# Performance work log

Measured on AMD Instinct MI355X. Metric: run time of the kernel, lower is better.

## Reference

```python
import jax, jax.numpy as jnp
import numpy as np

d_model = 512


def setup_inputs() -> dict:
    key = jax.random.key(0)
    k1, k2, k3, k4 = jax.random.split(key, 4)
    B, T, d_k = 8, 2048, 64
    scale = 1.0 / np.sqrt(d_model)
    x = jax.random.normal(k1, (B, T, d_model), dtype=jnp.float32)
    Wk = jax.random.normal(k2, (d_model, d_k), dtype=jnp.float32) * scale
    Wq = jax.random.normal(k3, (d_model, d_k), dtype=jnp.float32) * scale
    Wv = jax.random.normal(k4, (d_model, d_k), dtype=jnp.float32) * scale
    return {"x": x, "Wk": Wk, "Wq": Wq, "Wv": Wv}


def reference(x, Wk, Wq, Wv):
    # x: [B,T,C]; W*: [C,d_k]  (torch Linear weight is [d_k,C]; we store transposed)
    k = jnp.einsum('btc,cd->btd', x, Wk)
    q = jnp.einsum('btc,cd->btd', x, Wq)
    v = jnp.einsum('btc,cd->btd', x, Wv)
    d_k = k.shape[-1]
    scores = jnp.einsum('bqd,bkd->bqk', q, k) / jnp.sqrt(jnp.float32(d_k))
    attn = jax.nn.softmax(scores, axis=-1)  # [B,T,T]
    return jnp.einsum('bqk,bkd->bqd', attn, v)
```

## Files before the change

### kernel.cpp

```cpp
#include <hip/hip_runtime.h>
#include <hip/hip_bf16.h>
#include <stdint.h>


typedef short bf16x8 __attribute__((ext_vector_type(8)));
typedef float f32x4 __attribute__((ext_vector_type(4)));

#define MFMA_BF16 __builtin_amdgcn_mfma_f32_16x16x32_bf16

__device__ __forceinline__ unsigned int pk2(float a, float b) {
    __hip_bfloat162 h = __float22bfloat162_rn(float2{a, b});
    union { __hip_bfloat162 h; unsigned int u; } r; r.h = h;
    return r.u;
}

__device__ __forceinline__ uint2 pack4_bf16(float a, float b, float c, float d) {
    uint2 r; r.x = pk2(a, b); r.y = pk2(c, d); return r;
}

__device__ __forceinline__ bf16x8 cvt8(f32x4 a, f32x4 b) {
    union { bf16x8 v; unsigned int u[4]; } r;
    r.u[0] = pk2(a[0], a[1]); r.u[1] = pk2(a[2], a[3]);
    r.u[2] = pk2(b[0], b[1]); r.u[3] = pk2(b[2], b[3]);
    return r.v;
}

__device__ __forceinline__ unsigned short bf1(float a) {
    __hip_bfloat16 h = __float2bfloat16(a);
    union { __hip_bfloat16 h; unsigned short u; } r; r.h = h;
    return r.u;
}

__global__ void prep_kernel(const float* __restrict__ x,
                            const float* __restrict__ Wq,
                            const float* __restrict__ Wk,
                            const float* __restrict__ Wv,
                            unsigned short* __restrict__ xb2,
                            unsigned short* __restrict__ wt2)
{
    if (blockIdx.x < 48) {
        int id = blockIdx.x * 256 + threadIdx.x;
        int c    = id & 15;
        int quad = (id >> 4) & 3;
        int ks   = (id >> 6) & 15;
        int mt   = (id >> 10) & 3;
        int w    = id >> 12;
        const float* src = (w == 0) ? Wq : ((w == 1) ? Wk : Wv);
        const int n  = mt * 16 + c;
        const int k0 = ks * 32 + quad * 8;
        unsigned short* dst = wt2 + (size_t)id * 8;
        #pragma unroll
        for (int j = 0; j < 8; j++)
            dst[j] = bf1(src[(size_t)(k0 + j) * 64 + n]);
        return;
    }
    int i = (blockIdx.x - 48) * 256 + threadIdx.x;
    int tok    = i >> 6;
    int dblock = i & 63;
    f32x4 a = *(const f32x4*)(x + (size_t)i * 8);
    f32x4 b = *(const f32x4*)(x + (size_t)i * 8 + 4);
    int tt = tok >> 4, c = tok & 15;
    int ks = dblock >> 2, quad = dblock & 3;
    size_t chunk = ((size_t)(tt * 16 + ks) * 4 + quad) * 16 + c;
    *(bf16x8*)(xb2 + chunk * 8) = cvt8(a, b);
}

__global__ __launch_bounds__(256, 1) void proj_kernel(
    const unsigned short* __restrict__ xb2, const unsigned short* __restrict__ wt2,
    unsigned short* __restrict__ qg, unsigned short* __restrict__ kg2,
    unsigned short* __restrict__ vg2)
{
    const int lane = threadIdx.x & 63;
    const int c    = lane & 15;
    const int quad = lane >> 4;
    const int wave = threadIdx.x >> 6;
    const int gw   = blockIdx.x * 4 + wave;
    const int w    = gw % 3;
    const int tt   = gw / 3;
    const int t0   = tt * 16;

    f32x4 acc[4];
    #pragma unroll
    for (int i = 0; i < 4; i++) acc[i] = f32x4{0.f, 0.f, 0.f, 0.f};

    const unsigned short* xbase = xb2 + ((size_t)tt * 16 * 64 + lane) * 8;
    const unsigned short* wbase = wt2 + ((size_t)w * 4 * 16 * 64 + lane) * 8;

    #pragma unroll 4
    for (int ks = 0; ks < 16; ks++) {
        bf16x8 xf = *(const bf16x8*)(xbase + (size_t)ks * 64 * 8);
        #pragma unroll
        for (int mt = 0; mt < 4; mt++) {
            bf16x8 wa = *(const bf16x8*)(wbase + ((size_t)mt * 16 + ks) * 64 * 8);
            acc[mt] = MFMA_BF16(wa, xf, acc[mt], 0, 0, 0);
        }
    }

    const int b  = t0 >> 11;
    const int tb = t0 & 2047;

    if (w == 0) {
        unsigned short* base = qg + (size_t)(t0 + c) * 64;
        #pragma unroll
        for (int mt = 0; mt < 4; mt++)
            *(uint2*)(base + mt * 16 + quad * 4) =
                pack4_bf16(acc[mt][0], acc[mt][1], acc[mt][2], acc[mt][3]);
    } else if (w == 1) {
        const int g = tb >> 4;
        #pragma unroll
        for (int mt = 0; mt < 4; mt++) {
            const int h  = mt >> 1;
            const int qk = (mt & 1) * 2 + (quad >> 1);
            size_t chunk = (size_t)b * 16384 + ((size_t)(g * 2 + h) * 4 + qk) * 16 + c;
            *(uint2*)(kg2 + chunk * 8 + (quad & 1) * 4) =
                pack4_bf16(acc[mt][0], acc[mt][1], acc[mt][2], acc[mt][3]);
        }
    } else {
        const int tk = tb + c;
        const int s  = tk >> 5;
        const int qv = (tk >> 3) & 3;
        const int j  = tk & 7;
        #pragma unroll
        for (int mt = 0; mt < 4; mt++) {
            size_t chunk = (size_t)b * 16384 + ((size_t)(s * 4 + mt) * 4 + qv) * 16 + quad * 4;
            unsigned short* dst = vg2 + chunk * 8 + j;
            dst[0]  = bf1(acc[mt][0]);
            dst[8]  = bf1(acc[mt][1]);
            dst[16] = bf1(acc[mt][2]);
            dst[24] = bf1(acc[mt][3]);
        }
    }
}

__global__ __launch_bounds__(256, 1) void attn_kernel(
    const unsigned short* __restrict__ qg, const unsigned short* __restrict__ kg2,
    const unsigned short* __restrict__ vg2, float* __restrict__ out)
{
    __shared__ unsigned short pt[4][2][16 * 136];
    __shared__ float obuf[4][2][16][68];
    __shared__ float lbuf[4][2][16];

    const int lane = threadIdx.x & 63;
    const int wave = threadIdx.x >> 6;
    const int c    = lane & 15;
    const int quad = lane >> 4;
    const int b    = blockIdx.x & 7;
    const int g    = blockIdx.x >> 3;
    const int tb   = b * 2048 + g * 32;

    unsigned short* ptw = &pt[wave][0][0];
    const unsigned short* kbase = kg2 + ((size_t)b * 16384 + lane) * 8;
    const unsigned short* vbase = vg2 + ((size_t)b * 16384 + lane) * 8;

    bf16x8 qa0 = *(const bf16x8*)(qg + (size_t)(tb + c) * 64 + quad * 8);
    bf16x8 qa1 = *(const bf16x8*)(qg + (size_t)(tb + c) * 64 + 32 + quad * 8);
    bf16x8 qc0 = *(const bf16x8*)(qg + (size_t)(tb + 16 + c) * 64 + quad * 8);
    bf16x8 qc1 = *(const bf16x8*)(qg + (size_t)(tb + 16 + c) * 64 + 32 + quad * 8);

    f32x4 oa0 = {0,0,0,0}, oa1 = {0,0,0,0}, oa2 = {0,0,0,0}, oa3 = {0,0,0,0};
    f32x4 ob0 = {0,0,0,0}, ob1 = {0,0,0,0}, ob2 = {0,0,0,0}, ob3 = {0,0,0,0};
    f32x4 laccA = {0,0,0,0}, laccB = {0,0,0,0};
    const float cexp = 0.18033688011112042f;

    for (int kt = wave * 4; kt < wave * 4 + 4; kt++) {
        const int key0 = kt * 128;
        const int g0   = key0 >> 4;
        const int s0   = key0 >> 5;

        f32x4 stA[8], stB[8];
        const f32x4 z = {0,0,0,0};
        #pragma unroll
        for (int mt = 0; mt < 8; mt++) {
            bf16x8 k0 = *(const bf16x8*)(kbase + (size_t)((g0 + mt) * 2    ) * 64 * 8);
            bf16x8 k1 = *(const bf16x8*)(kbase + (size_t)((g0 + mt) * 2 + 1) * 64 * 8);
            stA[mt] = MFMA_BF16(k0, qa0, z, 0, 0, 0);
            stA[mt] = MFMA_BF16(k1, qa1, stA[mt], 0, 0, 0);
            stB[mt] = MFMA_BF16(k0, qc0, z, 0, 0, 0);
            stB[mt] = MFMA_BF16(k1, qc1, stB[mt], 0, 0, 0);
        }

        bf16x8 va[2][4];
        #pragma unroll
        for (int mt = 0; mt < 4; mt++) {
            va[0][mt] = *(const bf16x8*)(vbase + (size_t)((s0    ) * 4 + mt) * 64 * 8);
            va[1][mt] = *(const bf16x8*)(vbase + (size_t)((s0 + 1) * 4 + mt) * 64 * 8);
        }

        asm volatile("" ::: "memory");
        #pragma unroll
        for (int mt = 0; mt < 8; mt++) {
            float p0 = __builtin_amdgcn_exp2f(stA[mt][0] * cexp);
            float p1 = __builtin_amdgcn_exp2f(stA[mt][1] * cexp);
            float p2 = __builtin_amdgcn_exp2f(stA[mt][2] * cexp);
            float p3 = __builtin_amdgcn_exp2f(stA[mt][3] * cexp);
            laccA[0] += p0; laccA[1] += p1; laccA[2] += p2; laccA[3] += p3;
            *(uint2*)(ptw + c * 136 + mt * 16 + quad * 4) = pack4_bf16(p0, p1, p2, p3);
        }
        #pragma unroll
        for (int mt = 0; mt < 8; mt++) {
            float p0 = __builtin_amdgcn_exp2f(stB[mt][0] * cexp);
            float p1 = __builtin_amdgcn_exp2f(stB[mt][1] * cexp);
            float p2 = __builtin_amdgcn_exp2f(stB[mt][2] * cexp);
            float p3 = __builtin_amdgcn_exp2f(stB[mt][3] * cexp);
            laccB[0] += p0; laccB[1] += p1; laccB[2] += p2; laccB[3] += p3;
            *(uint2*)(ptw + 2176 + c * 136 + mt * 16 + quad * 4) = pack4_bf16(p0, p1, p2, p3);
        }
        asm volatile("" ::: "memory");

        #pragma unroll
        for (int ks = 0; ks < 4; ks++) {
            bf16x8 pbA = *(const bf16x8*)(ptw + c * 136 + ks * 32 + quad * 8);
            bf16x8 pbB = *(const bf16x8*)(ptw + 2176 + c * 136 + ks * 32 + quad * 8);
            bf16x8 v0 = va[ks & 1][0], v1 = va[ks & 1][1];
            bf16x8 v2 = va[ks & 1][2], v3 = va[ks & 1][3];
            if (ks < 2) {
                #pragma unroll
                for (int mt = 0; mt < 4; mt++)
                    va[ks & 1][mt] =
                        *(const bf16x8*)(vbase + (size_t)((s0 + ks + 2) * 4 + mt) * 64 * 8);
            }
            oa0 = MFMA_BF16(v0, pbA, oa0, 0, 0, 0);
            oa1 = MFMA_BF16(v1, pbA, oa1, 0, 0, 0);
            oa2 = MFMA_BF16(v2, pbA, oa2, 0, 0, 0);
            oa3 = MFMA_BF16(v3, pbA, oa3, 0, 0, 0);
            ob0 = MFMA_BF16(v0, pbB, ob0, 0, 0, 0);
            ob1 = MFMA_BF16(v1, pbB, ob1, 0, 0, 0);
            ob2 = MFMA_BF16(v2, pbB, ob2, 0, 0, 0);
            ob3 = MFMA_BF16(v3, pbB, ob3, 0, 0, 0);
        }
        asm volatile("" ::: "memory");
    }

    float lA = (laccA[0] + laccA[1]) + (laccA[2] + laccA[3]);
    lA += __shfl_xor(lA, 16);
    lA += __shfl_xor(lA, 32);
    float lB = (laccB[0] + laccB[1]) + (laccB[2] + laccB[3]);
    lB += __shfl_xor(lB, 16);
    lB += __shfl_xor(lB, 32);

    *(f32x4*)&obuf[wave][0][c][ 0 + quad * 4] = oa0;
    *(f32x4*)&obuf[wave][0][c][16 + quad * 4] = oa1;
    *(f32x4*)&obuf[wave][0][c][32 + quad * 4] = oa2;
    *(f32x4*)&obuf[wave][0][c][48 + quad * 4] = oa3;
    *(f32x4*)&obuf[wave][1][c][ 0 + quad * 4] = ob0;
    *(f32x4*)&obuf[wave][1][c][16 + quad * 4] = ob1;
    *(f32x4*)&obuf[wave][1][c][32 + quad * 4] = ob2;
    *(f32x4*)&obuf[wave][1][c][48 + quad * 4] = ob3;
    if (quad == 0) { lbuf[wave][0][c] = lA; lbuf[wave][1][c] = lB; }
    __syncthreads();

    const int tid = threadIdx.x;
    const int row = tid >> 3;
    const int d0  = (tid & 7) * 8;
    const int qt  = row >> 4;
    const int r   = row & 15;
    const float L = (lbuf[0][qt][r] + lbuf[1][qt][r]) +
                    (lbuf[2][qt][r] + lbuf[3][qt][r]);
    const float rl = 1.f / L;
    f32x4 Oa = {0,0,0,0}, Ob = {0,0,0,0};
    #pragma unroll
    for (int w = 0; w < 4; w++) {
        f32x4 a = *(const f32x4*)&obuf[w][qt][r][d0];
        f32x4 bfr = *(const f32x4*)&obuf[w][qt][r][d0 + 4];
        Oa[0] += a[0]; Oa[1] += a[1]; Oa[2] += a[2]; Oa[3] += a[3];
        Ob[0] += bfr[0]; Ob[1] += bfr[1]; Ob[2] += bfr[2]; Ob[3] += bfr[3];
    }
    Oa[0] *= rl; Oa[1] *= rl; Oa[2] *= rl; Oa[3] *= rl;
    Ob[0] *= rl; Ob[1] *= rl; Ob[2] *= rl; Ob[3] *= rl;
    float* op = out + (size_t)(tb + row) * 64 + d0;
    *(f32x4*)op       = Oa;
    *(f32x4*)(op + 4) = Ob;
}

extern "C" void kernel_launch(void* const* d_in, const int* in_sizes, int n_in,
                              void* d_out, int out_size, void* d_ws, size_t ws_size,
                              hipStream_t stream)
{
    const float* x  = (const float*)d_in[0];
    const float* Wk = (const float*)d_in[1];
    const float* Wq = (const float*)d_in[2];
    const float* Wv = (const float*)d_in[3];
    float* out = (float*)d_out;

    char* ws = (char*)d_ws;
    unsigned short* qg  = (unsigned short*)(ws);
    unsigned short* kg2 = (unsigned short*)(ws + (2u << 20));
    unsigned short* vg2 = (unsigned short*)(ws + (4u << 20));
    unsigned short* wt2 = (unsigned short*)(ws + (6u << 20));
    unsigned short* xb2 = (unsigned short*)(ws + (7u << 20));

    hipLaunchKernelGGL(prep_kernel, dim3(4144), dim3(256), 0, stream,
                       x, Wq, Wk, Wv, xb2, wt2);
    hipLaunchKernelGGL(proj_kernel, dim3(768),  dim3(256), 0, stream,
                       xb2, wt2, qg, kg2, vg2);
    hipLaunchKernelGGL(attn_kernel, dim3(512),  dim3(256), 0, stream,
                       qg, kg2, vg2, out);
}
```

Measured before the change: 112.0 us.

## Fuse x bf16 conversion into projection kernel via swizzled LDS staging

The separate pass that converted x to bf16 and wrote a tiled copy to global memory is removed. Each projection block now loads its 16 tokens of fp32 x directly, converts them into a bank-swizzled shared-memory tile, and its four waves each compute three of the twelve Q/K/V output fragments from that tile. This drops the round trip of the bf16 x copy through global memory and lets the x tile be reused across Q, K and V within one block. The cost is a block-wide barrier and LDS traffic in the projection, plus a different work split (1024 blocks, three accumulators per wave).

```diff
diff --git a/kernel.cpp b/kernel.cpp
--- a/kernel.cpp
+++ b/kernel.cpp
@@ -31,103 +31,100 @@
     return r.u;
 }
 
-__global__ void prep_kernel(const float* __restrict__ x,
-                            const float* __restrict__ Wq,
-                            const float* __restrict__ Wk,
-                            const float* __restrict__ Wv,
-                            unsigned short* __restrict__ xb2,
-                            unsigned short* __restrict__ wt2)
-{
-    if (blockIdx.x < 48) {
-        int id = blockIdx.x * 256 + threadIdx.x;
-        int c    = id & 15;
-        int quad = (id >> 4) & 3;
-        int ks   = (id >> 6) & 15;
-        int mt   = (id >> 10) & 3;
-        int w    = id >> 12;
-        const float* src = (w == 0) ? Wq : ((w == 1) ? Wk : Wv);
-        const int n  = mt * 16 + c;
-        const int k0 = ks * 32 + quad * 8;
-        unsigned short* dst = wt2 + (size_t)id * 8;
-        #pragma unroll
-        for (int j = 0; j < 8; j++)
-            dst[j] = bf1(src[(size_t)(k0 + j) * 64 + n]);
-        return;
-    }
-    int i = (blockIdx.x - 48) * 256 + threadIdx.x;
-    int tok    = i >> 6;
-    int dblock = i & 63;
-    f32x4 a = *(const f32x4*)(x + (size_t)i * 8);
-    f32x4 b = *(const f32x4*)(x + (size_t)i * 8 + 4);
-    int tt = tok >> 4, c = tok & 15;
-    int ks = dblock >> 2, quad = dblock & 3;
-    size_t chunk = ((size_t)(tt * 16 + ks) * 4 + quad) * 16 + c;
-    *(bf16x8*)(xb2 + chunk * 8) = cvt8(a, b);
+__global__ void wt_kernel(const float* __restrict__ Wq,
+                          const float* __restrict__ Wk,
+                          const float* __restrict__ Wv,
+                          unsigned short* __restrict__ wt2)
+{
+    int id = blockIdx.x * 256 + threadIdx.x;
+    int c    = id & 15;
+    int quad = (id >> 4) & 3;
+    int ks   = (id >> 6) & 15;
+    int mt   = (id >> 10) & 3;
+    int w    = id >> 12;
+    const float* src = (w == 0) ? Wq : ((w == 1) ? Wk : Wv);
+    const int n  = mt * 16 + c;
+    const int k0 = ks * 32 + quad * 8;
+    unsigned short* dst = wt2 + (size_t)id * 8;
+    #pragma unroll
+    for (int j = 0; j < 8; j++)
+        dst[j] = bf1(src[(size_t)(k0 + j) * 64 + n]);
 }
 
 __global__ __launch_bounds__(256, 1) void proj_kernel(
-    const unsigned short* __restrict__ xb2, const unsigned short* __restrict__ wt2,
+    const float* __restrict__ x, const unsigned short* __restrict__ wt2,
     unsigned short* __restrict__ qg, unsigned short* __restrict__ kg2,
     unsigned short* __restrict__ vg2)
 {
-    const int lane = threadIdx.x & 63;
+    __shared__ unsigned short xs[8192];
+
+    const int tid  = threadIdx.x;
+    const int lane = tid & 63;
+    const int wave = tid >> 6;
     const int c    = lane & 15;
     const int quad = lane >> 4;
-    const int wave = threadIdx.x >> 6;
-    const int gw   = blockIdx.x * 4 + wave;
-    const int w    = gw % 3;
-    const int tt   = gw / 3;
+    const int tt   = blockIdx.x;
     const int t0   = tt * 16;
 
-    f32x4 acc[4];
-    #pragma unroll
-    for (int i = 0; i < 4; i++) acc[i] = f32x4{0.f, 0.f, 0.f, 0.f};
-
-    const unsigned short* xbase = xb2 + ((size_t)tt * 16 * 64 + lane) * 8;
-    const unsigned short* wbase = wt2 + ((size_t)w * 4 * 16 * 64 + lane) * 8;
-
+    const float* xb = x + (size_t)tt * 8192;
+    #pragma unroll
+    for (int t = 0; t < 4; t++) {
+        int i = t * 256 + tid;
+        f32x4 a = *(const f32x4*)(xb + (size_t)i * 8);
+        f32x4 b = *(const f32x4*)(xb + (size_t)i * 8 + 4);
+        int tok = i >> 6;
+        int db  = i & 63;
+        *(bf16x8*)(xs + db * 128 + ((tok ^ (db & 7)) * 8)) = cvt8(a, b);
+    }
+    __syncthreads();
+
+    f32x4 acc[3];
+    #pragma unroll
+    for (int r = 0; r < 3; r++) acc[r] = f32x4{0.f, 0.f, 0.f, 0.f};
+
+    const int fbase = wave * 3;
     #pragma unroll 4
     for (int ks = 0; ks < 16; ks++) {
-        bf16x8 xf = *(const bf16x8*)(xbase + (size_t)ks * 64 * 8);
-        #pragma unroll
-        for (int mt = 0; mt < 4; mt++) {
-            bf16x8 wa = *(const bf16x8*)(wbase + ((size_t)mt * 16 + ks) * 64 * 8);
-            acc[mt] = MFMA_BF16(wa, xf, acc[mt], 0, 0, 0);
+        bf16x8 xf = *(const bf16x8*)(
+            xs + ks * 512 + quad * 128 + ((c ^ ((ks * 4 + quad) & 7)) * 8));
+        #pragma unroll
+        for (int r = 0; r < 3; r++) {
+            int f = fbase + r;
+            bf16x8 wa = *(const bf16x8*)(wt2 + ((size_t)(f * 16 + ks) * 64 + lane) * 8);
+            acc[r] = MFMA_BF16(wa, xf, acc[r], 0, 0, 0);
         }
     }
 
     const int b  = t0 >> 11;
     const int tb = t0 & 2047;
 
-    if (w == 0) {
-        unsigned short* base = qg + (size_t)(t0 + c) * 64;
-        #pragma unroll
-        for (int mt = 0; mt < 4; mt++)
+    #pragma unroll
+    for (int r = 0; r < 3; r++) {
+        const int f  = fbase + r;
+        const int w  = f >> 2;
+        const int mt = f & 3;
+        if (w == 0) {
+            unsigned short* base = qg + (size_t)(t0 + c) * 64;
             *(uint2*)(base + mt * 16 + quad * 4) =
-                pack4_bf16(acc[mt][0], acc[mt][1], acc[mt][2], acc[mt][3]);
-    } else if (w == 1) {
-        const int g = tb >> 4;
-        #pragma unroll
-        for (int mt = 0; mt < 4; mt++) {
+                pack4_bf16(acc[r][0], acc[r][1], acc[r][2], acc[r][3]);
+        } else if (w == 1) {
+            const int g  = tb >> 4;
             const int h  = mt >> 1;
             const int qk = (mt & 1) * 2 + (quad >> 1);
             size_t chunk = (size_t)b * 16384 + ((size_t)(g * 2 + h) * 4 + qk) * 16 + c;
             *(uint2*)(kg2 + chunk * 8 + (quad & 1) * 4) =
-                pack4_bf16(acc[mt][0], acc[mt][1], acc[mt][2], acc[mt][3]);
-        }
-    } else {
-        const int tk = tb + c;
-        const int s  = tk >> 5;
-        const int qv = (tk >> 3) & 3;
-        const int j  = tk & 7;
-        #pragma unroll
-        for (int mt = 0; mt < 4; mt++) {
+                pack4_bf16(acc[r][0], acc[r][1], acc[r][2], acc[r][3]);
+        } else {
+            const int tk = tb + c;
+            const int s  = tk >> 5;
+            const int qv = (tk >> 3) & 3;
+            const int j  = tk & 7;
             size_t chunk = (size_t)b * 16384 + ((size_t)(s * 4 + mt) * 4 + qv) * 16 + quad * 4;
             unsigned short* dst = vg2 + chunk * 8 + j;
-            dst[0]  = bf1(acc[mt][0]);
-            dst[8]  = bf1(acc[mt][1]);
-            dst[16] = bf1(acc[mt][2]);
-            dst[24] = bf1(acc[mt][3]);
+            dst[0]  = bf1(acc[r][0]);
+            dst[8]  = bf1(acc[r][1]);
+            dst[16] = bf1(acc[r][2]);
+            dst[24] = bf1(acc[r][3]);
         }
     }
 }
@@ -287,12 +284,11 @@
     unsigned short* kg2 = (unsigned short*)(ws + (2u << 20));
     unsigned short* vg2 = (unsigned short*)(ws + (4u << 20));
     unsigned short* wt2 = (unsigned short*)(ws + (6u << 20));
-    unsigned short* xb2 = (unsigned short*)(ws + (7u << 20));
-
-    hipLaunchKernelGGL(prep_kernel, dim3(4144), dim3(256), 0, stream,
-                       x, Wq, Wk, Wv, xb2, wt2);
-    hipLaunchKernelGGL(proj_kernel, dim3(768),  dim3(256), 0, stream,
-                       xb2, wt2, qg, kg2, vg2);
+
+    hipLaunchKernelGGL(wt_kernel,   dim3(48),   dim3(256), 0, stream,
+                       Wq, Wk, Wv, wt2);
+    hipLaunchKernelGGL(proj_kernel, dim3(1024), dim3(256), 0, stream,
+                       x, wt2, qg, kg2, vg2);
     hipLaunchKernelGGL(attn_kernel, dim3(512),  dim3(256), 0, stream,
                        qg, kg2, vg2, out);
 }
```

Measured after the change: 109.3 us. -2.3%, faster.
